# Performance work log

Hardware: AMD Instinct MI355X
Metric: run time of the kernel (lower is better)

Reference implementation:

```python
import jax, jax.numpy as jnp
import numpy as np

B, T, D, H = 8, 1024, 1024, 16
HD = D // H  # per-head dim = 64


def setup_inputs() -> dict:
    key = jax.random.key(0)
    ks = jax.random.split(key, 9)
    s = 1.0 / np.sqrt(D)
    return {
        "x": jax.random.normal(ks[0], (B, T, D), dtype=jnp.float32),
        "y": jax.random.normal(ks[1], (B, T, D), dtype=jnp.float32),
        "Wq": jax.random.normal(ks[2], (D, D), dtype=jnp.float32) * s,
        "Wk": jax.random.normal(ks[3], (D, D), dtype=jnp.float32) * s,
        "Wv": jax.random.normal(ks[4], (D, D), dtype=jnp.float32) * s,
        "Wox": jax.random.normal(ks[5], (D, D), dtype=jnp.float32) * s,
        "box": jnp.zeros((D,), dtype=jnp.float32),
        "Woy": jax.random.normal(ks[6], (D, D), dtype=jnp.float32) * s,
        "boy": jnp.zeros((D,), dtype=jnp.float32),
    }


def _split_heads(t):
    # (B, T, D) -> (B, H, T, HD)
    return t.reshape(B, T, H, HD).transpose(0, 2, 1, 3)


def _merge_heads(t):
    # (B, H, T, HD) -> (B, T, D)
    return t.transpose(0, 2, 1, 3).reshape(B, T, D)


def reference(x, y, Wq, Wk, Wv, Wox, box, Woy, boy):
    # Shared Q/K/V projections applied cross-wise (torch Linear: t @ W.T)
    q_sx = _split_heads(y @ Wq.T)  # queries from y attend over x
    k_sx = _split_heads(x @ Wk.T)
    v_sx = _split_heads(x @ Wv.T)
    q_sy = _split_heads(x @ Wq.T)  # queries from x attend over y
    k_sy = _split_heads(y @ Wk.T)
    v_sy = _split_heads(y @ Wv.T)

    scale = jnp.sqrt(jnp.asarray(HD, dtype=x.dtype))
    scores_x = jnp.einsum('bhqd,bhkd->bhqk', q_sx, k_sx)
    scores_y = jnp.einsum('bhqd,bhkd->bhqk', q_sy, k_sy)
    # cat on head dim + reshape(B,2,H,T,T) + mean over dim 1 == per-head average
    attn = jax.nn.softmax((scores_x + scores_y) * (0.5 / scale), axis=-1)

    out1 = _merge_heads(jnp.einsum('bhqk,bhkd->bhqd', attn, v_sx))
    out2 = _merge_heads(jnp.einsum('bhqk,bhkd->bhqd', attn, v_sy))
    out1 = out1 @ Wox.T + box
    out2 = out2 @ Woy.T + boy
    return (out1, out2)
```

## Files before the change

kernel.cpp:

```cpp
#include <hip/hip_runtime.h>
#include <stdint.h>

#define DEV __device__ __forceinline__

typedef __bf16 bf16x8 __attribute__((ext_vector_type(8)));
typedef __bf16 bf16x4 __attribute__((ext_vector_type(4)));
typedef short s16x4 __attribute__((ext_vector_type(4)));
typedef float f32x4 __attribute__((ext_vector_type(4)));
typedef unsigned short u16;
typedef u16 u16x4v __attribute__((ext_vector_type(4)));
typedef u16 u16x8 __attribute__((ext_vector_type(8)));
typedef uint32_t u32;

static constexpr int Bb = 8, Tt = 1024, Dd = 1024, Hh = 16;
static constexpr int BT = Bb * Tt;

DEV u16 f2bf(float f) {
  u32 u = __float_as_uint(f);
  u32 r = (u + 0x7FFFu + ((u >> 16) & 1u)) >> 16;
  return (u16)r;
}
DEV u32 cvtpk(float lo, float hi) {
  u32 r;
  asm("v_cvt_pk_bf16_f32 %0, %1, %2" : "=v"(r) : "v"(lo), "v"(hi));
  return r;
}
DEV void gload_lds16(const void* g, void* lds) {
  __builtin_amdgcn_global_load_lds(
      (const __attribute__((address_space(1))) void*)g,
      (__attribute__((address_space(3))) void*)lds,
      16, 0, 0);
}
DEV f32x4 MFMA16(bf16x4 a, bf16x4 b, f32x4 c) {
#if __has_builtin(__builtin_amdgcn_mfma_f32_16x16x16_bf16)
  return __builtin_amdgcn_mfma_f32_16x16x16_bf16(a, b, c, 0, 0, 0);
#elif __has_builtin(__builtin_amdgcn_mfma_f32_16x16x16bf16_1k)
  union { bf16x4 b; s16x4 s; } ua, ub;
  ua.b = a; ub.b = b;
  return __builtin_amdgcn_mfma_f32_16x16x16bf16_1k(ua.s, ub.s, c, 0, 0, 0);
#else
  asm("v_mfma_f32_16x16x16_bf16 %0, %1, %2, %0" : "+v"(c) : "v"(a), "v"(b));
  return c;
#endif
}

__global__ __launch_bounds__(256) void k_cvt2(const float* __restrict__ x,
                                              const float* __restrict__ y,
                                              u16* __restrict__ xb, u16* __restrict__ yb) {
  const float* src = blockIdx.z ? y : x;
  u16* dst = blockIdx.z ? yb : xb;
  const int n8 = BT * Dd / 8;
  int i = blockIdx.x * blockDim.x + threadIdx.x;
  int stride = gridDim.x * blockDim.x;
  for (; i < n8; i += stride) {
    const float4* p = reinterpret_cast<const float4*>(src) + (size_t)i * 2;
    float4 a = p[0], b = p[1];
    u16x8 o;
    o[0] = f2bf(a.x); o[1] = f2bf(a.y); o[2] = f2bf(a.z); o[3] = f2bf(a.w);
    o[4] = f2bf(b.x); o[5] = f2bf(b.y); o[6] = f2bf(b.z); o[7] = f2bf(b.w);
    reinterpret_cast<u16x8*>(dst)[i] = o;
  }
}

__global__ __launch_bounds__(256) void k_cvt5(const float* __restrict__ a0,
                                              const float* __restrict__ a1,
                                              const float* __restrict__ a2,
                                              const float* __restrict__ a3,
                                              const float* __restrict__ a4,
                                              u16* __restrict__ Wb) {
  int z = blockIdx.z;
  const float* src = (z == 0) ? a0 : (z == 1) ? a1 : (z == 2) ? a2 : (z == 3) ? a3 : a4;
  u16* dst = Wb + (size_t)z * (Dd * Dd);
  int i = blockIdx.x * blockDim.x + threadIdx.x;
  const float4* p = reinterpret_cast<const float4*>(src) + (size_t)i * 2;
  float4 a = p[0], b = p[1];
  u16x8 o;
  o[0] = f2bf(a.x); o[1] = f2bf(a.y); o[2] = f2bf(a.z); o[3] = f2bf(a.w);
  o[4] = f2bf(b.x); o[5] = f2bf(b.y); o[6] = f2bf(b.z); o[7] = f2bf(b.w);
  reinterpret_cast<u16x8*>(dst)[i] = o;
}

template <int MODE, int GX, int GY>
__global__ __launch_bounds__(512, 2) void k_gemm256(
    const u16* __restrict__ xb, const u16* __restrict__ yb,
    const u16* __restrict__ W0,
    u16* __restrict__ Qb, u16* __restrict__ Kb, u16* __restrict__ Vtg,
    const float* __restrict__ bx, const float* __restrict__ by,
    float* __restrict__ out) {
  __shared__ alignas(16) u16 As[2][256 * 64];
  __shared__ alignas(16) u16 Bs[2][256 * 64];
  const int tid = threadIdx.x;
  const int l = tid & 63, wid = tid >> 6;
  const int wr = wid >> 2, wc = wid & 3;

  constexpr int NWG = GX * GY * 2;
  const int d0b = blockIdx.x;
  const int wk = (d0b & 7) * (NWG / 8) + (d0b >> 3);
  const int tz = wk / (GX * GY);
  const int rr = wk % (GX * GY);
  const int ty = rr / GX, tx = rr % GX;
  const int m0 = ty * 256, n0 = tx * 256;

  const u16* Ag;
  const u16* Wg;
  if constexpr (MODE == 0) {
    Ag = tz ? yb : xb;
    Wg = W0;
  } else {
    Ag = xb + tz * 64;
    Wg = W0 + (size_t)tz * (Dd * Dd);
  }

  auto stageA = [&](int buf, int kt, int half) {
#pragma unroll
    for (int i = 0; i < 2; ++i) {
      int idx = i * 512 + tid;
      int row = idx >> 3, P = idx & 7, G = P ^ (row & 7);
      const u16* src;
      if constexpr (MODE == 0) {
        src = Ag + (size_t)(m0 + half * 128 + row) * 1024 + kt * 64 + G * 8;
      } else {
        int m = m0 + half * 128 + row;
        src = Ag + ((size_t)((m >> 10) * 16 + kt) * 1024 + (m & 1023)) * 128 + G * 8;
      }
      gload_lds16(src, &As[buf][half * 8192 + idx * 8]);
    }
  };
  auto stageB = [&](int buf, int kt, int half) {
#pragma unroll
    for (int i = 0; i < 2; ++i) {
      int idx = i * 512 + tid;
      int row = idx >> 3, P = idx & 7, G = P ^ (row & 7);
      gload_lds16(Wg + (size_t)(n0 + half * 128 + row) * 1024 + kt * 64 + G * 8,
                  &Bs[buf][half * 8192 + idx * 8]);
    }
  };
  auto ldA = [&](int b, int m, int kk) -> bf16x8 {
    int row = wr * 128 + m * 16 + (l & 15);
    int P = (kk * 4 + (l >> 4)) ^ (row & 7);
    return *reinterpret_cast<const bf16x8*>(&As[b][row * 64 + P * 8]);
  };
  auto ldB = [&](int b, int n, int kk) -> bf16x8 {
    int row = wc * 64 + n * 16 + (l & 15);
    int P = (kk * 4 + (l >> 4)) ^ (row & 7);
    return *reinterpret_cast<const bf16x8*>(&Bs[b][row * 64 + P * 8]);
  };

  f32x4 acc[8][4] = {};

  stageA(0, 0, 0); stageB(0, 0, 0); stageA(0, 0, 1); stageB(0, 0, 1);
  asm volatile("s_waitcnt vmcnt(0)" ::: "memory");
  __builtin_amdgcn_s_barrier();

  for (int kt = 0; kt < 16; ++kt) {
    const int b = kt & 1, nb = b ^ 1;
    const bool pf = (kt < 15);
    bf16x8 bfr[4][2], afr[2][2];

#define QUAD(p)                                                                     \
  do {                                                                              \
    __builtin_amdgcn_s_barrier();                                                   \
    asm volatile("s_waitcnt lgkmcnt(0)" ::: "memory");                              \
    __builtin_amdgcn_sched_barrier(0);                                              \
    __builtin_amdgcn_s_setprio(1);                                                  \
    _Pragma("unroll") for (int mm = 0; mm < 2; ++mm)                                \
        _Pragma("unroll") for (int n = 0; n < 4; ++n)                               \
            _Pragma("unroll") for (int kk = 0; kk < 2; ++kk)                        \
                acc[2 * (p) + mm][n] = __builtin_amdgcn_mfma_f32_16x16x32_bf16(     \
                    afr[mm][kk], bfr[n][kk], acc[2 * (p) + mm][n], 0, 0, 0);        \
    __builtin_amdgcn_s_setprio(0);                                                  \
  } while (0)

#pragma unroll
    for (int n = 0; n < 4; ++n) { bfr[n][0] = ldB(b, n, 0); bfr[n][1] = ldB(b, n, 1); }
    afr[0][0] = ldA(b, 0, 0); afr[0][1] = ldA(b, 0, 1);
    afr[1][0] = ldA(b, 1, 0); afr[1][1] = ldA(b, 1, 1);
    if (pf) { stageA(nb, kt + 1, 0); stageB(nb, kt + 1, 0); }
    QUAD(0);
    __builtin_amdgcn_s_barrier();

    afr[0][0] = ldA(b, 2, 0); afr[0][1] = ldA(b, 2, 1);
    afr[1][0] = ldA(b, 3, 0); afr[1][1] = ldA(b, 3, 1);
    if (pf) { stageA(nb, kt + 1, 1); stageB(nb, kt + 1, 1); }
    QUAD(1);
    __builtin_amdgcn_s_barrier();

    afr[0][0] = ldA(b, 4, 0); afr[0][1] = ldA(b, 4, 1);
    afr[1][0] = ldA(b, 5, 0); afr[1][1] = ldA(b, 5, 1);
    QUAD(2);
    __builtin_amdgcn_s_barrier();

    afr[0][0] = ldA(b, 6, 0); afr[0][1] = ldA(b, 6, 1);
    afr[1][0] = ldA(b, 7, 0); afr[1][1] = ldA(b, 7, 1);
    QUAD(3);
    asm volatile("s_waitcnt vmcnt(0)" ::: "memory");
    __builtin_amdgcn_s_barrier();
#undef QUAD
  }

#pragma unroll
  for (int m = 0; m < 8; ++m)
#pragma unroll
    for (int n = 0; n < 4; ++n) {
      int rb = m0 + wr * 128 + m * 16 + (l >> 4) * 4;
      int col = n0 + wc * 64 + n * 16 + (l & 15);
      if constexpr (MODE == 0) {
        int proj = col >> 10;
        int slot = ((proj == 0) ? 1 : 0) ^ tz;
        int bh = ((rb >> 10) << 4) + ((col >> 6) & 15);
        int t0 = rb & 1023;
        int dc = col & 63;
        if (proj == 2) {
          int newoff = (t0 >> 5) * 32 + ((t0 >> 2) & 3) * 8 + ((t0 >> 4) & 1) * 4;
          u16x4v pk;
#pragma unroll
          for (int j = 0; j < 4; ++j) pk[j] = f2bf(acc[m][n][j]);
          *reinterpret_cast<u16x4v*>(Vtg + (size_t)bh * 131072 +
                                     (size_t)(slot * 64 + dc) * 1024 + newoff) = pk;
        } else {
          float sc = (proj == 0) ? 0.09016994f : 1.0f;
          u16* dstp = (proj ? Kb : Qb) + (size_t)bh * 131072 + (size_t)t0 * 128 + slot * 64 + dc;
#pragma unroll
          for (int j = 0; j < 4; ++j) dstp[(size_t)j * 128] = f2bf(acc[m][n][j] * sc);
        }
      } else {
        const float* bias = tz ? by : bx;
        float* dstp = out + (size_t)tz * BT * Dd;
        float bv = bias[col];
#pragma unroll
        for (int j = 0; j < 4; ++j)
          dstp[(size_t)(rb + j) * 1024 + col] = acc[m][n][j] + bv;
      }
    }
}

__global__ __launch_bounds__(512, 4) void k_attn(const u16* __restrict__ Q,
                                                 const u16* __restrict__ K,
                                                 const u16* __restrict__ Vt,
                                                 u16* __restrict__ O) {
  __shared__ alignas(16) u16 Ks[2][8192];
  __shared__ alignas(16) u16 Vs[2][8192];
  const int tid = threadIdx.x;
  const int l = tid & 63, w = tid >> 6;
  const int bid = blockIdx.x;
  const int xcd = bid & 7, li = bid >> 3;
  const int bh = xcd + 8 * (li & 15);
  const int qblk = li >> 4;
  const int q0 = qblk * 128 + w * 16;
  const size_t base = (size_t)bh * 131072;

  bf16x8 qf[4];
#pragma unroll
  for (int dc = 0; dc < 4; ++dc)
    qf[dc] = *reinterpret_cast<const bf16x8*>(
        Q + base + (size_t)(q0 + (l & 15)) * 128 + dc * 32 + (l >> 4) * 8);

  const u16* kp[2];
  const u16* vp[2];
#pragma unroll
  for (int i = 0; i < 2; ++i) {
    int idx = i * 512 + tid;
    {
      int dc = idx >> 8, kv = (idx >> 2) & 63, pp = idx & 3, g = pp ^ ((kv >> 1) & 3);
      kp[i] = K + base + (size_t)kv * 128 + dc * 32 + g * 8;
    }
    {
      int c = idx >> 9, d = (idx >> 2) & 127, pp = idx & 3, g = pp ^ ((d >> 1) & 3);
      vp[i] = Vt + base + (size_t)d * 1024 + c * 32 + g * 8;
    }
  }
  const int i0 = tid * 8, i1 = (512 + tid) * 8;

  const int koff = (l & 15) * 32 + (((l >> 4) ^ (((l & 15) >> 1) & 3))) * 8;

  auto stage = [&](int buf, int kv0) {
    gload_lds16(kp[0] + (size_t)kv0 * 128, &Ks[buf][i0]);
    gload_lds16(kp[1] + (size_t)kv0 * 128, &Ks[buf][i1]);
    gload_lds16(vp[0] + kv0, &Vs[buf][i0]);
    gload_lds16(vp[1] + kv0, &Vs[buf][i1]);
  };

  float m_run = -3e38f, l_run = 0.f;
  f32x4 Oa[8] = {};

  stage(0, 0);
  __syncthreads();

  for (int t16 = 0; t16 < 16; ++t16) {
    const int cur = t16 & 1;
    if (t16 < 15) stage(cur ^ 1, (t16 + 1) * 64);

    f32x4 S[4];
    __builtin_amdgcn_s_setprio(1);
#pragma unroll
    for (int t = 0; t < 4; ++t) {
      f32x4 s = {};
#pragma unroll
      for (int dc = 0; dc < 4; ++dc) {
        bf16x8 kb = *reinterpret_cast<const bf16x8*>(&Ks[cur][dc * 2048 + t * 512 + koff]);
        s = __builtin_amdgcn_mfma_f32_16x16x32_bf16(kb, qf[dc], s, 0, 0, 0);
      }
      S[t] = s;
    }
    __builtin_amdgcn_s_setprio(0);

    float mxl = fmaxf(fmaxf(fmaxf(S[0][0], S[0][1]), fmaxf(S[0][2], S[0][3])),
                      fmaxf(fmaxf(S[1][0], S[1][1]), fmaxf(S[1][2], S[1][3])));
    float mx2 = fmaxf(fmaxf(fmaxf(S[2][0], S[2][1]), fmaxf(S[2][2], S[2][3])),
                      fmaxf(fmaxf(S[3][0], S[3][1]), fmaxf(S[3][2], S[3][3])));
    mxl = fmaxf(mxl, mx2);

    const int grow = __any(mxl > m_run + 11.0f);
    float mn = m_run, alpha = 1.0f;
    if (grow) {
      float mx = fmaxf(mxl, __shfl_xor(mxl, 16));
      mx = fmaxf(mx, __shfl_xor(mx, 32));
      mn = fmaxf(m_run, mx);
      alpha = __builtin_exp2f(m_run - mn);
      m_run = mn;
    }
    float rs = 0.f;
#pragma unroll
    for (int t = 0; t < 4; ++t)
#pragma unroll
      for (int j = 0; j < 4; ++j) {
        S[t][j] = __builtin_exp2f(S[t][j] - mn);
        rs += S[t][j];
      }
    rs += __shfl_xor(rs, 16);
    rs += __shfl_xor(rs, 32);
    if (grow) {
      l_run = alpha * l_run + rs;
#pragma unroll
      for (int n = 0; n < 8; ++n) Oa[n] *= alpha;
    } else {
      l_run += rs;
    }

    union { u32 w2[2]; bf16x4 v; } pb[4];
#pragma unroll
    for (int t = 0; t < 4; ++t) {
      pb[t].w2[0] = cvtpk(S[t][0], S[t][1]);
      pb[t].w2[1] = cvtpk(S[t][2], S[t][3]);
    }

    asm volatile("s_nop 1");
    __builtin_amdgcn_s_setprio(1);
#pragma unroll
    for (int c = 0; c < 2; ++c)
#pragma unroll
      for (int n = 0; n < 8; ++n) {
        bf16x8 av = *reinterpret_cast<const bf16x8*>(&Vs[cur][c * 4096 + n * 512 + koff]);
        bf16x4 a0 = __builtin_shufflevector(av, av, 0, 1, 2, 3);
        bf16x4 a1 = __builtin_shufflevector(av, av, 4, 5, 6, 7);
        Oa[n] = MFMA16(a0, pb[2 * c].v, Oa[n]);
        Oa[n] = MFMA16(a1, pb[2 * c + 1].v, Oa[n]);
      }
    __builtin_amdgcn_s_setprio(0);

    __syncthreads();
  }
  asm volatile("s_nop 7");

  float inv = 1.0f / l_run;
#pragma unroll
  for (int n = 0; n < 8; ++n) {
    u16x4v pk;
#pragma unroll
    for (int j = 0; j < 4; ++j) pk[j] = f2bf(Oa[n][j] * inv);
    *reinterpret_cast<u16x4v*>(
        O + base + (size_t)(q0 + (l & 15)) * 128 + n * 16 + (l >> 4) * 4) = pk;
  }
}

extern "C" void kernel_launch(void* const* d_in, const int* in_sizes, int n_in,
                              void* d_out, int out_size, void* d_ws, size_t ws_size,
                              hipStream_t stream) {
  const float* x   = (const float*)d_in[0];
  const float* y   = (const float*)d_in[1];
  const float* Wq  = (const float*)d_in[2];
  const float* Wk  = (const float*)d_in[3];
  const float* Wv  = (const float*)d_in[4];
  const float* Wox = (const float*)d_in[5];
  const float* box = (const float*)d_in[6];
  const float* Woy = (const float*)d_in[7];
  const float* boy = (const float*)d_in[8];

  u16* ws = (u16*)d_ws;
  size_t off = 0;
  u16* xb  = ws + off; off += (size_t)BT * Dd;
  u16* yb  = ws + off; off += (size_t)BT * Dd;
  u16* Wqb = ws + off; off += (size_t)Dd * Dd;
  u16* Wkb = ws + off; off += (size_t)Dd * Dd;
  u16* Wvb = ws + off; off += (size_t)Dd * Dd;
  u16* Woxb = ws + off; off += (size_t)Dd * Dd;
  u16* Woyb = ws + off; off += (size_t)Dd * Dd;
  (void)Wkb; (void)Wvb; (void)Woyb;
  const size_t attn_elems = (size_t)Bb * Hh * Tt * 128;
  u16* Qb = ws + off; off += attn_elems;
  u16* Kb = ws + off; off += attn_elems;
  u16* Vb = ws + off; off += attn_elems;
  u16* Ob = ws + off; off += attn_elems;

  k_cvt2<<<dim3(1024, 1, 2), dim3(256), 0, stream>>>(x, y, xb, yb);
  k_cvt5<<<dim3(512, 1, 5), dim3(256), 0, stream>>>(Wq, Wk, Wv, Wox, Woy, Wqb);

  k_gemm256<0, 12, 32><<<dim3(768), dim3(512), 0, stream>>>(
      xb, yb, Wqb, Qb, Kb, Vb, nullptr, nullptr, nullptr);

  k_attn<<<dim3(1024), dim3(512), 0, stream>>>(Qb, Kb, Vb, Ob);

  k_gemm256<1, 4, 32><<<dim3(256), dim3(512), 0, stream>>>(
      Ob, nullptr, Woxb, nullptr, nullptr, nullptr, box, boy, (float*)d_out);
}
```

Before: 276.2 us.

## Reschedule GEMM main loop into quadrant MMA blocks with finer vmcnt waits

Reorganizes the projection GEMM inner loop into four 4x2 MFMA quadrants and remaps the A/B staging so each prefetch half covers the rows those quadrants read. Global-to-LDS prefetches for the next k-tile spread across all four phases, and partial vmcnt waits replace the full drain at the end of each iteration. This is meant to overlap memory transfers with MFMA work and cut stall time at the iteration boundary. It adds barriers per phase, and the ordering of the partial waits must be correct to avoid reading LDS before it is filled.

```diff
diff --git a/kernel.cpp b/kernel.cpp
--- a/kernel.cpp
+++ b/kernel.cpp
@@ -111,28 +111,32 @@
     Wg = W0 + (size_t)tz * (Dd * Dd);
   }
 
-  auto stageA = [&](int buf, int kt, int half) {
+  auto stageA = [&](int buf, int kt, int h) {
 #pragma unroll
     for (int i = 0; i < 2; ++i) {
       int idx = i * 512 + tid;
-      int row = idx >> 3, P = idx & 7, G = P ^ (row & 7);
+      int rh = idx >> 3, P = idx & 7;
+      int row = (rh & 63) + h * 64 + (rh >> 6) * 128;
+      int G = P ^ (row & 7);
       const u16* src;
       if constexpr (MODE == 0) {
-        src = Ag + (size_t)(m0 + half * 128 + row) * 1024 + kt * 64 + G * 8;
+        src = Ag + (size_t)(m0 + row) * 1024 + kt * 64 + G * 8;
       } else {
-        int m = m0 + half * 128 + row;
+        int m = m0 + row;
         src = Ag + ((size_t)((m >> 10) * 16 + kt) * 1024 + (m & 1023)) * 128 + G * 8;
       }
-      gload_lds16(src, &As[buf][half * 8192 + idx * 8]);
+      gload_lds16(src, &As[buf][row * 64 + P * 8]);
     }
   };
-  auto stageB = [&](int buf, int kt, int half) {
+  auto stageB = [&](int buf, int kt, int h) {
 #pragma unroll
     for (int i = 0; i < 2; ++i) {
       int idx = i * 512 + tid;
-      int row = idx >> 3, P = idx & 7, G = P ^ (row & 7);
-      gload_lds16(Wg + (size_t)(n0 + half * 128 + row) * 1024 + kt * 64 + G * 8,
-                  &Bs[buf][half * 8192 + idx * 8]);
+      int rh = idx >> 3, P = idx & 7;
+      int row = (rh & 31) + h * 32 + (rh >> 5) * 64;
+      int G = P ^ (row & 7);
+      gload_lds16(Wg + (size_t)(n0 + row) * 1024 + kt * 64 + G * 8,
+                  &Bs[buf][row * 64 + P * 8]);
     }
   };
   auto ldA = [&](int b, int m, int kk) -> bf16x8 {
@@ -152,51 +156,56 @@
   asm volatile("s_waitcnt vmcnt(0)" ::: "memory");
   __builtin_amdgcn_s_barrier();
 
-  for (int kt = 0; kt < 16; ++kt) {
-    const int b = kt & 1, nb = b ^ 1;
-    const bool pf = (kt < 15);
-    bf16x8 bfr[4][2], afr[2][2];
-
-#define QUAD(p)                                                                     \
+#define MMQ(MO, NO)                                                                 \
   do {                                                                              \
     __builtin_amdgcn_s_barrier();                                                   \
     asm volatile("s_waitcnt lgkmcnt(0)" ::: "memory");                              \
     __builtin_amdgcn_sched_barrier(0);                                              \
     __builtin_amdgcn_s_setprio(1);                                                  \
-    _Pragma("unroll") for (int mm = 0; mm < 2; ++mm)                                \
-        _Pragma("unroll") for (int n = 0; n < 4; ++n)                               \
+    _Pragma("unroll") for (int mm = 0; mm < 4; ++mm)                                \
+        _Pragma("unroll") for (int nn = 0; nn < 2; ++nn)                            \
             _Pragma("unroll") for (int kk = 0; kk < 2; ++kk)                        \
-                acc[2 * (p) + mm][n] = __builtin_amdgcn_mfma_f32_16x16x32_bf16(     \
-                    afr[mm][kk], bfr[n][kk], acc[2 * (p) + mm][n], 0, 0, 0);        \
+                acc[(MO) + mm][(NO) + nn] = __builtin_amdgcn_mfma_f32_16x16x32_bf16(\
+                    afr[mm][kk], bfr2[nn][kk], acc[(MO) + mm][(NO) + nn], 0, 0, 0); \
     __builtin_amdgcn_s_setprio(0);                                                  \
+    __builtin_amdgcn_s_barrier();                                                   \
   } while (0)
 
-#pragma unroll
-    for (int n = 0; n < 4; ++n) { bfr[n][0] = ldB(b, n, 0); bfr[n][1] = ldB(b, n, 1); }
-    afr[0][0] = ldA(b, 0, 0); afr[0][1] = ldA(b, 0, 1);
-    afr[1][0] = ldA(b, 1, 0); afr[1][1] = ldA(b, 1, 1);
-    if (pf) { stageA(nb, kt + 1, 0); stageB(nb, kt + 1, 0); }
-    QUAD(0);
-    __builtin_amdgcn_s_barrier();
-
-    afr[0][0] = ldA(b, 2, 0); afr[0][1] = ldA(b, 2, 1);
-    afr[1][0] = ldA(b, 3, 0); afr[1][1] = ldA(b, 3, 1);
-    if (pf) { stageA(nb, kt + 1, 1); stageB(nb, kt + 1, 1); }
-    QUAD(1);
-    __builtin_amdgcn_s_barrier();
-
-    afr[0][0] = ldA(b, 4, 0); afr[0][1] = ldA(b, 4, 1);
-    afr[1][0] = ldA(b, 5, 0); afr[1][1] = ldA(b, 5, 1);
-    QUAD(2);
-    __builtin_amdgcn_s_barrier();
-
-    afr[0][0] = ldA(b, 6, 0); afr[0][1] = ldA(b, 6, 1);
-    afr[1][0] = ldA(b, 7, 0); afr[1][1] = ldA(b, 7, 1);
-    QUAD(3);
-    asm volatile("s_waitcnt vmcnt(0)" ::: "memory");
-    __builtin_amdgcn_s_barrier();
-#undef QUAD
-  }
+  for (int kt = 0; kt < 16; ++kt) {
+    const int b = kt & 1, nb = b ^ 1;
+    const bool pf = kt < 15;
+    bf16x8 afr[4][2], bfr2[2][2];
+
+    asm volatile("s_waitcnt vmcnt(4)" ::: "memory");
+#pragma unroll
+    for (int m = 0; m < 4; ++m) { afr[m][0] = ldA(b, m, 0); afr[m][1] = ldA(b, m, 1); }
+#pragma unroll
+    for (int n = 0; n < 2; ++n) { bfr2[n][0] = ldB(b, n, 0); bfr2[n][1] = ldB(b, n, 1); }
+    if (pf) stageA(nb, kt + 1, 0);
+    MMQ(0, 0);
+
+    if (pf) asm volatile("s_waitcnt vmcnt(4)" ::: "memory");
+    else    asm volatile("s_waitcnt vmcnt(2)" ::: "memory");
+#pragma unroll
+    for (int m = 0; m < 4; ++m) { afr[m][0] = ldA(b, 4 + m, 0); afr[m][1] = ldA(b, 4 + m, 1); }
+    if (pf) stageB(nb, kt + 1, 0);
+    MMQ(4, 0);
+
+    if (pf) asm volatile("s_waitcnt vmcnt(4)" ::: "memory");
+    else    asm volatile("s_waitcnt vmcnt(0)" ::: "memory");
+#pragma unroll
+    for (int m = 0; m < 4; ++m) { afr[m][0] = ldA(b, m, 0); afr[m][1] = ldA(b, m, 1); }
+#pragma unroll
+    for (int n = 0; n < 2; ++n) { bfr2[n][0] = ldB(b, 2 + n, 0); bfr2[n][1] = ldB(b, 2 + n, 1); }
+    if (pf) stageA(nb, kt + 1, 1);
+    MMQ(0, 2);
+
+#pragma unroll
+    for (int m = 0; m < 4; ++m) { afr[m][0] = ldA(b, 4 + m, 0); afr[m][1] = ldA(b, 4 + m, 1); }
+    if (pf) stageB(nb, kt + 1, 1);
+    MMQ(4, 2);
+  }
+#undef MMQ
 
 #pragma unroll
   for (int m = 0; m < 8; ++m)
```

Result: no change. 281.0 us (+1.8%).
